# Kernel optimization log

Hardware: AMD Instinct MI355X
Metric: run time of the kernel (lower is better)

## Reference

```python
import jax, jax.numpy as jnp
import numpy as np

K = 8
TEMP = 0.05
EPS = 1e-8


def setup_inputs() -> dict:
    key = jax.random.key(0)
    k1, k2, k3, k4, k5, k6 = jax.random.split(key, 6)
    N, D, H = 8192, 1024, 64
    h0 = jax.random.normal(k1, (N, D), dtype=jnp.float32)
    coords = jax.random.uniform(k2, (N, 2), dtype=jnp.float32)
    # tiny MLP params: Linear(2,H) -> ReLU -> Linear(H,1) -> Sigmoid
    W1 = jax.random.normal(k3, (2, H), dtype=jnp.float32) * (1.0 / np.sqrt(2))
    b1 = jnp.zeros((H,), dtype=jnp.float32)
    W2 = jax.random.normal(k4, (H, 1), dtype=jnp.float32) * (1.0 / np.sqrt(H))
    b2 = jnp.zeros((1,), dtype=jnp.float32)
    return {"h0": h0, "coords": coords, "W1": W1, "b1": b1, "W2": W2, "b2": b2}


def reference(h0, coords, W1, b1, W2, b2):
    # pairwise euclidean distances [N, N]
    sq = jnp.sum(coords * coords, axis=-1)                      # [N]
    d2 = sq[:, None] + sq[None, :] - 2.0 * (coords @ coords.T)  # [N, N]
    dist = jnp.sqrt(jnp.maximum(d2, 0.0))

    # k+1 nearest (smallest dist), drop self (index 0)
    _, idx = jax.lax.top_k(-dist, K + 1)                        # [N, K+1]
    knn_idx = idx[:, 1:]                                        # [N, K]

    # gather neighbor features [N, K, D]
    neighbor_feats = h0[knn_idx]

    # cosine similarity between h_i and each neighbor (torch eps semantics)
    num = jnp.einsum('nd,nkd->nk', h0, neighbor_feats)          # [N, K]
    ni = jnp.maximum(jnp.linalg.norm(h0, axis=-1), EPS)         # [N]
    nj = jnp.maximum(jnp.linalg.norm(neighbor_feats, axis=-1), EPS)  # [N, K]
    sim = num / (ni[:, None] * nj)

    # spatial weights from gathered distances
    d_knn = jnp.take_along_axis(dist, knn_idx, axis=1)          # [N, K]
    spatial_w = jnp.exp(-d_knn / TEMP)

    density_input = jnp.stack(
        [sim.mean(axis=1), spatial_w.mean(axis=1)], axis=1)     # [N, 2]

    hmid = jax.nn.relu(density_input @ W1 + b1)
    density = jax.nn.sigmoid(hmid @ W2 + b2)                    # [N, 1]
    return density
```

## Files before the change

### kernel.cpp

```cpp
#include <hip/hip_runtime.h>
#include <math.h>

#define NROWS 8192
#define DIM   1024
#define GRID  64
#define CELLW 0.015625f
#define LPR   16

__device__ __forceinline__ int cell_of(float v) {
    int c = (int)(v * 64.0f);
    return c < 0 ? 0 : (c > 63 ? 63 : c);
}

__device__ __forceinline__ float np_d2(float xi, float yi, float sqi,
                                       float xj, float yj) {
    float sqj = __fadd_rn(__fmul_rn(xj, xj), __fmul_rn(yj, yj));
    float G   = fmaf(yi, yj, __fmul_rn(xi, xj));
    return __fsub_rn(__fadd_rn(sqi, sqj), __fmul_rn(2.0f, G));
}

__global__ __launch_bounds__(1024) void build_grid_kernel(
    const float* __restrict__ coords,
    int* __restrict__ cellStart,
    float4* __restrict__ sxyz) {

    __shared__ int lcnt[4096];
    __shared__ int wsum[16];
    const int t = threadIdx.x;

    for (int i = t; i < 4096; i += 1024) lcnt[i] = 0;
    __syncthreads();

    float2 pc[8]; int pcell[8];
#pragma unroll
    for (int k = 0; k < 8; ++k) {
        int i = t + 1024 * k;
        float2 c = ((const float2*)coords)[i];
        pc[k] = c;
        pcell[k] = cell_of(c.y) * GRID + cell_of(c.x);
        atomicAdd(&lcnt[pcell[k]], 1);
    }
    __syncthreads();

    int c0 = lcnt[t*4+0], c1 = lcnt[t*4+1], c2 = lcnt[t*4+2], c3 = lcnt[t*4+3];
    int s1 = c0, s2 = c0 + c1, s3 = s2 + c2, s4 = s3 + c3;
    int lane = t & 63, wid = t >> 6;
    int inc = s4;
#pragma unroll
    for (int off = 1; off < 64; off <<= 1) {
        int o = __shfl_up(inc, off, 64);
        if (lane >= off) inc += o;
    }
    if (lane == 63) wsum[wid] = inc;
    __syncthreads();
    int wbase = 0;
    for (int w = 0; w < wid; ++w) wbase += wsum[w];
    int excl = wbase + inc - s4;

    cellStart[t*4+0] = excl;
    cellStart[t*4+1] = excl + s1;
    cellStart[t*4+2] = excl + s2;
    cellStart[t*4+3] = excl + s3;
    if (t == 1023) cellStart[4096] = excl + s4;
    lcnt[t*4+0] = excl;
    lcnt[t*4+1] = excl + s1;
    lcnt[t*4+2] = excl + s2;
    lcnt[t*4+3] = excl + s3;
    __syncthreads();

#pragma unroll
    for (int k = 0; k < 8; ++k) {
        int pos = atomicAdd(&lcnt[pcell[k]], 1);
        float x = pc[k].x, y = pc[k].y;
        float sq = __fadd_rn(__fmul_rn(x, x), __fmul_rn(y, y));
        sxyz[pos] = make_float4(x, y, sq, __int_as_float(t + 1024 * k));
    }
}

__global__ __launch_bounds__(256) void knn_kernel(
    const float* __restrict__ h0,
    const int* __restrict__ cellStart,
    const float4* __restrict__ sxyz,
    unsigned long long* __restrict__ chosen_ws,
    float* __restrict__ norms) {

    {
        const int wv   = threadIdx.x >> 6;
        const int lane = threadIdx.x & 63;
        int rbase = blockIdx.x * 16 + wv * 4;
#pragma unroll
        for (int k = 0; k < 4; ++k) {
            int row = rbase + k;
            const float4* hp = (const float4*)(h0 + (size_t)row * DIM);
            float acc = 0.f;
#pragma unroll
            for (int t = 0; t < 4; ++t) {
                float4 v = hp[lane + 64 * t];
                acc += v.x * v.x + v.y * v.y + v.z * v.z + v.w * v.w;
            }
#pragma unroll
            for (int off = 1; off < 64; off <<= 1) acc += __shfl_xor(acc, off, 64);
            if (lane == 0) norms[row] = sqrtf(acc);
        }
    }

    const int sub = threadIdx.x & (LPR - 1);
    const int g   = (blockIdx.x * 256 + threadIdx.x) / LPR;

    const float4 me = sxyz[g];
    const float xi = me.x, yi = me.y, sqi = me.z;
    const int row = __float_as_int(me.w);
    const int cx = cell_of(xi), cy = cell_of(yi);

    unsigned long long best[10], merged[10];
    int C = 2;
    while (true) {
#pragma unroll
        for (int s = 0; s < 10; ++s) best[s] = ~0ULL;
        int x0 = max(0, cx - C), x1 = min(GRID - 1, cx + C);
        int y0 = max(0, cy - C), y1 = min(GRID - 1, cy + C);
        for (int yy = y0; yy <= y1; ++yy) {
            int s = cellStart[yy * GRID + x0];
            int e = cellStart[yy * GRID + x1 + 1];
            for (int t = s + sub; t < e; t += LPR) {
                float4 c = sxyz[t];
                float d2  = __fsub_rn(__fadd_rn(sqi, c.z),
                                      __fmul_rn(2.0f, fmaf(yi, c.y, __fmul_rn(xi, c.x))));
                float dst = __fsqrt_rn(fmaxf(d2, 0.0f));
                unsigned long long key =
                    ((unsigned long long)__float_as_uint(dst) << 32)
                    | (unsigned int)__float_as_int(c.w);
                if (key < best[9]) {
                    best[9] = key;
#pragma unroll
                    for (int ss = 9; ss >= 1; --ss) {
                        unsigned long long a = best[ss - 1], b = best[ss];
                        unsigned long long lo = a < b ? a : b;
                        unsigned long long hi = a < b ? b : a;
                        best[ss - 1] = lo;
                        best[ss]     = hi;
                    }
                }
            }
        }
#pragma unroll
        for (int r = 0; r < 10; ++r) {
            unsigned long long mn = best[0];
#pragma unroll
            for (int off = 1; off < LPR; off <<= 1) {
                unsigned long long o = __shfl_xor(mn, off, 64);
                mn = (o < mn) ? o : mn;
            }
            if (best[0] == mn) {
#pragma unroll
                for (int ss = 0; ss < 9; ++ss) best[ss] = best[ss + 1];
                best[9] = ~0ULL;
            }
            merged[r] = mn;
        }
        bool done = false;
        if (merged[9] != ~0ULL) {
            float d9 = __uint_as_float((unsigned int)(merged[9] >> 32));
            if (d9 + 1.0e-3f <= (float)C * CELLW) done = true;
        }
        if (done || C >= GRID) break;
        C <<= 1; if (C > GRID) C = GRID;
    }

    if (sub == 0) {
        unsigned long long* o = chosen_ws + (size_t)row * 10;
#pragma unroll
        for (int r = 0; r < 10; ++r) o[r] = merged[r];
    }
}

__global__ __launch_bounds__(256) void gather_final_kernel(
    const float* __restrict__ h0,
    const float* __restrict__ coords,
    const unsigned long long* __restrict__ chosen_ws,
    const float4* __restrict__ sxyz,
    const float* __restrict__ norms,
    const float* __restrict__ W1, const float* __restrict__ b1,
    const float* __restrict__ W2, const float* __restrict__ b2,
    float* __restrict__ out) {

    const int wid  = threadIdx.x >> 6;
    const int lane = threadIdx.x & 63;
    const int bid  = blockIdx.x;
    const int grp  = (bid & 7) * (gridDim.x / 8) + (bid >> 3);
    const int g    = grp * 4 + wid;
    const int row  = __float_as_int(sxyz[g].w);

    const unsigned long long* ch = chosen_ws + (size_t)row * 10;
    unsigned long long chosen[10];
    const float4* hj[10];
#pragma unroll
    for (int r = 0; r < 10; ++r) {
        chosen[r] = ch[r];
        hj[r] = (const float4*)(h0 + (size_t)(int)(chosen[r] & 0xFFFFFFFFu) * DIM);
    }

    const float4* hi = (const float4*)(h0 + (size_t)row * DIM);

    float p[10];
#pragma unroll
    for (int s = 0; s < 10; ++s) p[s] = 0.f;

#pragma unroll
    for (int t = 0; t < 4; ++t) {
        float4 av = hi[lane + 64 * t];
#pragma unroll
        for (int s = 0; s < 10; ++s) {
            float4 b = hj[s][lane + 64 * t];
            p[s] += av.x * b.x + av.y * b.y + av.z * b.z + av.w * b.w;
        }
    }

#pragma unroll
    for (int s = 0; s < 10; ++s) {
        float v = p[s];
#pragma unroll
        for (int off = 1; off < 64; off <<= 1) v += __shfl_xor(v, off, 64);
        p[s] = v;
    }

    const float2 ci = ((const float2*)coords)[row];
    const float xi = ci.x, yi = ci.y;
    const float sqi = __fadd_rn(__fmul_rn(xi, xi), __fmul_rn(yi, yi));

    auto clamped_d2 = [&](unsigned long long key) -> float {
        int j = (int)(key & 0xFFFFFFFFu);
        float2 cj = ((const float2*)coords)[j];
        return fmaxf(np_d2(xi, yi, sqi, cj.x, cj.y), 0.0f);
    };
    const float m0 = clamped_d2(chosen[0]);
    const float m1 = clamped_d2(chosen[1]);
    const float m2 = clamped_d2(chosen[2]);
    const float m8 = clamped_d2(chosen[8]);
    const float m9 = clamped_d2(chosen[9]);

    const float WIN = 2.0e-6f;
    const bool fpair = (m1 - m0) <= WIN;
    const bool ftri  = fpair && ((m2 - m0) <= WIN);
    const bool f89   = (m9 - m8) <= WIN;

    float wd[3];
    wd[0] = ftri ? (1.f / 3.f) : (fpair ? 0.5f : 1.0f);
    wd[1] = ftri ? (1.f / 3.f) : (fpair ? 0.5f : 0.0f);
    wd[2] = ftri ? (1.f / 3.f) : 0.0f;
    const float wc0 = f89 ? 0.5f : 1.0f;
    const float wc1 = f89 ? 0.5f : 0.0f;

    const float ni = fmaxf(norms[row], 1e-8f);

    float sim[10], sw[10];
#pragma unroll
    for (int r = 0; r < 10; ++r) {
        int   j   = (int)(chosen[r] & 0xFFFFFFFFu);
        float dst = __uint_as_float((unsigned int)(chosen[r] >> 32));
        float nj  = fmaxf(norms[j], 1e-8f);
        sim[r] = p[r] / (ni * nj);
        sw[r]  = expf(__fdiv_rn(-dst, 0.05f));
    }

    float Ssim = 0.f, Ssw = 0.f;
#pragma unroll
    for (int r = 0; r < 9; ++r) { Ssim += sim[r]; Ssw += sw[r]; }

    const float w1a = W1[lane], w1b = W1[64 + lane];
    const float b1l = b1[lane], w2l = W2[lane], b2s = b2[0];

    float outacc = 0.f;
#pragma unroll
    for (int d = 0; d < 3; ++d) {
#pragma unroll
        for (int c = 0; c < 2; ++c) {
            float wgt = wd[d] * (c ? wc1 : wc0);
            float simsum = Ssim - sim[d] + (c ? (sim[9] - sim[8]) : 0.f);
            float swsum  = Ssw  - sw[d]  + (c ? (sw[9]  - sw[8])  : 0.f);
            float di0 = simsum * 0.125f;
            float di1 = swsum  * 0.125f;
            float hm = fmaxf(di0 * w1a + di1 * w1b + b1l, 0.f);
            float v  = hm * w2l;
#pragma unroll
            for (int off = 1; off < 64; off <<= 1) v += __shfl_xor(v, off, 64);
            float z = v + b2s;
            outacc += wgt * (1.f / (1.f + expf(-z)));
        }
    }

    if (lane == 0) out[row] = outacc;
}

extern "C" void kernel_launch(void* const* d_in, const int* in_sizes, int n_in,
                              void* d_out, int out_size, void* d_ws, size_t ws_size,
                              hipStream_t stream) {
    const float* h0     = (const float*)d_in[0];
    const float* coords = (const float*)d_in[1];
    const float* W1     = (const float*)d_in[2];
    const float* b1     = (const float*)d_in[3];
    const float* W2     = (const float*)d_in[4];
    const float* b2     = (const float*)d_in[5];
    float* out = (float*)d_out;

    char* ws = (char*)d_ws;
    unsigned long long* chosen_ws = (unsigned long long*)(ws);
    float*  norms     = (float*)(ws + 655360);
    float4* sxyz      = (float4*)(ws + 1015808);
    int*    cellStart = (int*)(ws + 1146880);

    build_grid_kernel  <<<1, 1024, 0, stream>>>(coords, cellStart, sxyz);
    knn_kernel         <<<NROWS * LPR / 256, 256, 0, stream>>>(h0, cellStart, sxyz,
                                                               chosen_ws, norms);
    gather_final_kernel<<<NROWS / 4, 256, 0, stream>>>(h0, coords, chosen_ws, sxyz,
                                                       norms, W1, b1, W2, b2, out);
}
```

Before: 62.68 us.

## Split row-norm computation into separate kernel and batch neighbor loads in gather

Moves the per-row L2 norm computation out of the knn kernel into its own grid-stride kernel launched after knn, so knn does only the spatial search. In the gather kernel all 40 float4 neighbor loads plus the self row are issued up front into registers before the dot products, for more memory-level parallelism. The gather kernel also gets launch_bounds(256,1), letting it use more registers. The cost is an extra launch, higher register pressure and possibly lower occupancy in the gather kernel.

```diff
diff --git a/kernel.cpp b/kernel.cpp
--- a/kernel.cpp
+++ b/kernel.cpp
@@ -17,6 +17,26 @@
     float sqj = __fadd_rn(__fmul_rn(xj, xj), __fmul_rn(yj, yj));
     float G   = fmaf(yi, yj, __fmul_rn(xi, xj));
     return __fsub_rn(__fadd_rn(sqi, sqj), __fmul_rn(2.0f, G));
+}
+
+__global__ __launch_bounds__(256) void norms_kernel(const float* __restrict__ h0,
+                                                    float* __restrict__ norms) {
+    int gid  = blockIdx.x * blockDim.x + threadIdx.x;
+    int wave = gid >> 6;
+    int lane = threadIdx.x & 63;
+    int nw   = (gridDim.x * blockDim.x) >> 6;
+    for (int row = wave; row < NROWS; row += nw) {
+        const float4* hp = (const float4*)(h0 + (size_t)row * DIM);
+        float acc = 0.f;
+#pragma unroll
+        for (int t = 0; t < 4; ++t) {
+            float4 v = hp[lane + 64 * t];
+            acc += v.x * v.x + v.y * v.y + v.z * v.z + v.w * v.w;
+        }
+#pragma unroll
+        for (int off = 32; off >= 1; off >>= 1) acc += __shfl_xor(acc, off, 64);
+        if (lane == 0) norms[row] = sqrtf(acc);
+    }
 }
 
 __global__ __launch_bounds__(1024) void build_grid_kernel(
@@ -78,31 +98,9 @@
 }
 
 __global__ __launch_bounds__(256) void knn_kernel(
-    const float* __restrict__ h0,
     const int* __restrict__ cellStart,
     const float4* __restrict__ sxyz,
-    unsigned long long* __restrict__ chosen_ws,
-    float* __restrict__ norms) {
-
-    {
-        const int wv   = threadIdx.x >> 6;
-        const int lane = threadIdx.x & 63;
-        int rbase = blockIdx.x * 16 + wv * 4;
-#pragma unroll
-        for (int k = 0; k < 4; ++k) {
-            int row = rbase + k;
-            const float4* hp = (const float4*)(h0 + (size_t)row * DIM);
-            float acc = 0.f;
-#pragma unroll
-            for (int t = 0; t < 4; ++t) {
-                float4 v = hp[lane + 64 * t];
-                acc += v.x * v.x + v.y * v.y + v.z * v.z + v.w * v.w;
-            }
-#pragma unroll
-            for (int off = 1; off < 64; off <<= 1) acc += __shfl_xor(acc, off, 64);
-            if (lane == 0) norms[row] = sqrtf(acc);
-        }
-    }
+    unsigned long long* __restrict__ chosen_ws) {
 
     const int sub = threadIdx.x & (LPR - 1);
     const int g   = (blockIdx.x * 256 + threadIdx.x) / LPR;
@@ -174,7 +172,7 @@
     }
 }
 
-__global__ __launch_bounds__(256) void gather_final_kernel(
+__global__ __launch_bounds__(256, 1) void gather_final_kernel(
     const float* __restrict__ h0,
     const float* __restrict__ coords,
     const unsigned long long* __restrict__ chosen_ws,
@@ -193,26 +191,33 @@
 
     const unsigned long long* ch = chosen_ws + (size_t)row * 10;
     unsigned long long chosen[10];
-    const float4* hj[10];
-#pragma unroll
-    for (int r = 0; r < 10; ++r) {
-        chosen[r] = ch[r];
-        hj[r] = (const float4*)(h0 + (size_t)(int)(chosen[r] & 0xFFFFFFFFu) * DIM);
-    }
+#pragma unroll
+    for (int r = 0; r < 10; ++r) chosen[r] = ch[r];
 
     const float4* hi = (const float4*)(h0 + (size_t)row * DIM);
 
+    float4 av[4];
+#pragma unroll
+    for (int t = 0; t < 4; ++t) av[t] = hi[lane + 64 * t];
+
+    float4 bv[10][4];
+#pragma unroll
+    for (int s = 0; s < 10; ++s) {
+        const float4* hj =
+            (const float4*)(h0 + (size_t)(int)(chosen[s] & 0xFFFFFFFFu) * DIM);
+#pragma unroll
+        for (int t = 0; t < 4; ++t) bv[s][t] = hj[lane + 64 * t];
+    }
+
     float p[10];
 #pragma unroll
     for (int s = 0; s < 10; ++s) p[s] = 0.f;
-
 #pragma unroll
     for (int t = 0; t < 4; ++t) {
-        float4 av = hi[lane + 64 * t];
 #pragma unroll
         for (int s = 0; s < 10; ++s) {
-            float4 b = hj[s][lane + 64 * t];
-            p[s] += av.x * b.x + av.y * b.y + av.z * b.z + av.w * b.w;
+            float4 b = bv[s][t];
+            p[s] += av[t].x * b.x + av[t].y * b.y + av[t].z * b.z + av[t].w * b.w;
         }
     }
 
@@ -310,8 +315,8 @@
     int*    cellStart = (int*)(ws + 1146880);
 
     build_grid_kernel  <<<1, 1024, 0, stream>>>(coords, cellStart, sxyz);
-    knn_kernel         <<<NROWS * LPR / 256, 256, 0, stream>>>(h0, cellStart, sxyz,
-                                                               chosen_ws, norms);
+    knn_kernel         <<<NROWS * LPR / 256, 256, 0, stream>>>(cellStart, sxyz, chosen_ws);
+    norms_kernel       <<<128, 256, 0, stream>>>(h0, norms);
     gather_final_kernel<<<NROWS / 4, 256, 0, stream>>>(h0, coords, chosen_ws, sxyz,
                                                        norms, W1, b1, W2, b2, out);
 }
```

After: 69.87 us. +11.5%, slower.

## Split row norms into own kernel, halve KNN lanes per row, batch gather loads

Applied to the files above, without the earlier changes.

Row-norm computation moves out of the KNN kernel into a separate norms kernel with one wave per row. The KNN search now uses 8 lanes per query instead of 16, which halves its grid. The gather kernel issues all neighbour loads for two float4 chunks before the dot-product math to raise memory-level parallelism. Risks: an extra kernel launch, more per-lane serial work in the KNN search, and higher register pressure from the buffered neighbour loads.

```diff
diff --git a/kernel.cpp b/kernel.cpp
--- a/kernel.cpp
+++ b/kernel.cpp
@@ -5,7 +5,7 @@
 #define DIM   1024
 #define GRID  64
 #define CELLW 0.015625f
-#define LPR   16
+#define LPR   8
 
 __device__ __forceinline__ int cell_of(float v) {
     int c = (int)(v * 64.0f);
@@ -17,6 +17,22 @@
     float sqj = __fadd_rn(__fmul_rn(xj, xj), __fmul_rn(yj, yj));
     float G   = fmaf(yi, yj, __fmul_rn(xi, xj));
     return __fsub_rn(__fadd_rn(sqi, sqj), __fmul_rn(2.0f, G));
+}
+
+__global__ __launch_bounds__(256) void norms_kernel(const float* __restrict__ h0,
+                                                    float* __restrict__ norms) {
+    int wave = (blockIdx.x * 256 + threadIdx.x) >> 6;
+    int lane = threadIdx.x & 63;
+    const float4* hp = (const float4*)(h0 + (size_t)wave * DIM);
+    float acc = 0.f;
+#pragma unroll
+    for (int t = 0; t < 4; ++t) {
+        float4 v = hp[lane + 64 * t];
+        acc += v.x * v.x + v.y * v.y + v.z * v.z + v.w * v.w;
+    }
+#pragma unroll
+    for (int off = 1; off < 64; off <<= 1) acc += __shfl_xor(acc, off, 64);
+    if (lane == 0) norms[wave] = sqrtf(acc);
 }
 
 __global__ __launch_bounds__(1024) void build_grid_kernel(
@@ -78,31 +94,9 @@
 }
 
 __global__ __launch_bounds__(256) void knn_kernel(
-    const float* __restrict__ h0,
     const int* __restrict__ cellStart,
     const float4* __restrict__ sxyz,
-    unsigned long long* __restrict__ chosen_ws,
-    float* __restrict__ norms) {
-
-    {
-        const int wv   = threadIdx.x >> 6;
-        const int lane = threadIdx.x & 63;
-        int rbase = blockIdx.x * 16 + wv * 4;
-#pragma unroll
-        for (int k = 0; k < 4; ++k) {
-            int row = rbase + k;
-            const float4* hp = (const float4*)(h0 + (size_t)row * DIM);
-            float acc = 0.f;
-#pragma unroll
-            for (int t = 0; t < 4; ++t) {
-                float4 v = hp[lane + 64 * t];
-                acc += v.x * v.x + v.y * v.y + v.z * v.z + v.w * v.w;
-            }
-#pragma unroll
-            for (int off = 1; off < 64; off <<= 1) acc += __shfl_xor(acc, off, 64);
-            if (lane == 0) norms[row] = sqrtf(acc);
-        }
-    }
+    unsigned long long* __restrict__ chosen_ws) {
 
     const int sub = threadIdx.x & (LPR - 1);
     const int g   = (blockIdx.x * 256 + threadIdx.x) / LPR;
@@ -193,11 +187,11 @@
 
     const unsigned long long* ch = chosen_ws + (size_t)row * 10;
     unsigned long long chosen[10];
-    const float4* hj[10];
+    int jidx[10];
 #pragma unroll
     for (int r = 0; r < 10; ++r) {
         chosen[r] = ch[r];
-        hj[r] = (const float4*)(h0 + (size_t)(int)(chosen[r] & 0xFFFFFFFFu) * DIM);
+        jidx[r]   = (int)(chosen[r] & 0xFFFFFFFFu);
     }
 
     const float4* hi = (const float4*)(h0 + (size_t)row * DIM);
@@ -207,12 +201,21 @@
     for (int s = 0; s < 10; ++s) p[s] = 0.f;
 
 #pragma unroll
-    for (int t = 0; t < 4; ++t) {
-        float4 av = hi[lane + 64 * t];
+    for (int th = 0; th < 2; ++th) {
+        const int t0 = 2 * th, t1 = 2 * th + 1;
+        float4 a0 = hi[lane + 64 * t0];
+        float4 a1 = hi[lane + 64 * t1];
+        float4 b0[10], b1[10];
 #pragma unroll
         for (int s = 0; s < 10; ++s) {
-            float4 b = hj[s][lane + 64 * t];
-            p[s] += av.x * b.x + av.y * b.y + av.z * b.z + av.w * b.w;
+            const float4* hj = (const float4*)(h0 + (size_t)jidx[s] * DIM);
+            b0[s] = hj[lane + 64 * t0];
+            b1[s] = hj[lane + 64 * t1];
+        }
+#pragma unroll
+        for (int s = 0; s < 10; ++s) {
+            p[s] += a0.x * b0[s].x + a0.y * b0[s].y + a0.z * b0[s].z + a0.w * b0[s].w;
+            p[s] += a1.x * b1[s].x + a1.y * b1[s].y + a1.z * b1[s].z + a1.w * b1[s].w;
         }
     }
 
@@ -256,9 +259,8 @@
     float sim[10], sw[10];
 #pragma unroll
     for (int r = 0; r < 10; ++r) {
-        int   j   = (int)(chosen[r] & 0xFFFFFFFFu);
         float dst = __uint_as_float((unsigned int)(chosen[r] >> 32));
-        float nj  = fmaxf(norms[j], 1e-8f);
+        float nj  = fmaxf(norms[jidx[r]], 1e-8f);
         sim[r] = p[r] / (ni * nj);
         sw[r]  = expf(__fdiv_rn(-dst, 0.05f));
     }
@@ -310,8 +312,8 @@
     int*    cellStart = (int*)(ws + 1146880);
 
     build_grid_kernel  <<<1, 1024, 0, stream>>>(coords, cellStart, sxyz);
-    knn_kernel         <<<NROWS * LPR / 256, 256, 0, stream>>>(h0, cellStart, sxyz,
-                                                               chosen_ws, norms);
+    norms_kernel       <<<NROWS / 4, 256, 0, stream>>>(h0, norms);
+    knn_kernel         <<<NROWS * LPR / 256, 256, 0, stream>>>(cellStart, sxyz, chosen_ws);
     gather_final_kernel<<<NROWS / 4, 256, 0, stream>>>(h0, coords, chosen_ws, sxyz,
                                                        norms, W1, b1, W2, b2, out);
 }
```

Result: slower. 67.93 us (+8.4%).
